# Kernel tuning notes

Hardware: AMD Instinct MI355X
Metric: run time of the kernel (lower is better)

## Reference

```python
import jax, jax.numpy as jnp
import numpy as np

WINDOW = 4  # window_size
H = 8       # n_heads


def setup_inputs() -> dict:
    key = jax.random.key(0)
    ks = jax.random.split(key, 12)
    B, C, T = 4, 512, 1024
    d = C // H
    x = jax.random.normal(ks[0], (B, C, T), dtype=jnp.float32)
    mask = jnp.ones((B, 1, 1, T), dtype=jnp.int32)
    s = 0.02
    Wq = jax.random.normal(ks[1], (C, C), dtype=jnp.float32) * s
    Wk = jax.random.normal(ks[2], (C, C), dtype=jnp.float32) * s
    Wv = jax.random.normal(ks[3], (C, C), dtype=jnp.float32) * s
    Wo = jax.random.normal(ks[4], (C, C), dtype=jnp.float32) * s
    bq = jnp.zeros((C,), jnp.float32)
    bk = jnp.zeros((C,), jnp.float32)
    bv = jnp.zeros((C,), jnp.float32)
    bo = jnp.zeros((C,), jnp.float32)
    rel_std = d ** (-0.5)
    emb_rel_k = jax.random.normal(ks[5], (1, 2 * WINDOW + 1, d), dtype=jnp.float32) * rel_std
    emb_rel_v = jax.random.normal(ks[6], (1, 2 * WINDOW + 1, d), dtype=jnp.float32) * rel_std
    return {"x": x, "mask": mask, "Wq": Wq, "bq": bq, "Wk": Wk, "bk": bk,
            "Wv": Wv, "bv": bv, "Wo": Wo, "bo": bo,
            "emb_rel_k": emb_rel_k, "emb_rel_v": emb_rel_v}


def _slice_rel_emb(emb, T, pad_len, start, end):
    # F.pad(emb, [0,0,pad,pad,0,0]) then [:, start:end] -> [1, 2T-1, d]
    p = jnp.pad(emb, ((0, 0), (pad_len, pad_len), (0, 0)))
    return p[:, start:end]


def reference(x, mask, Wq, bq, Wk, bk, Wv, bv, Wo, bo, emb_rel_k, emb_rel_v):
    B, C, T = x.shape
    d = C // H
    scale = jnp.asarray(np.sqrt(d), x.dtype)

    def proj(Wm, bm):
        return jnp.einsum('oc,bct->bot', Wm, x) + bm[None, :, None]

    def to_heads(t):  # [B,C,T] -> [B,H,T,d]
        return t.reshape(B, H, d, T).transpose(0, 1, 3, 2)

    query = to_heads(proj(Wq, bq))
    key_ = to_heads(proj(Wk, bk))
    value = to_heads(proj(Wv, bv))

    score = jnp.einsum('bhtd,bhsd->bhts', query, key_) / scale

    pad_len = max(0, T - (WINDOW + 1))
    start = max(0, WINDOW + 1 - T)
    end = start + 2 * T - 1

    k_emb = _slice_rel_emb(emb_rel_k, T, pad_len, start, end)  # [1, 2T-1, d]
    rel = jnp.einsum('bhtd,rd->bhtr', query, k_emb[0])          # [B,H,T,2T-1]
    # skew trick: relative -> absolute
    rel = jnp.pad(rel, ((0, 0), (0, 0), (0, 0), (0, 1))).reshape(B, H, 2 * T * T)
    rel = jnp.pad(rel, ((0, 0), (0, 0), (0, T - 1))).reshape(B, H, T + 1, 2 * T - 1)
    score_loc = rel[:, :, :T, T - 1:] / scale
    score = score + score_loc

    score = jnp.where(mask == 0, jnp.asarray(-10000.0, score.dtype), score)
    p_attn = jax.nn.softmax(score, axis=-1)  # dropout=0 (eval)

    output = jnp.einsum('bhts,bhsd->bhtd', p_attn, value)

    # inverse skew: absolute -> relative weights [B,H,T,2T-1]
    pw = jnp.pad(p_attn, ((0, 0), (0, 0), (0, 0), (0, T - 1))).reshape(B, H, T * (2 * T - 1))
    pw = jnp.pad(pw, ((0, 0), (0, 0), (T, 0))).reshape(B, H, T, 2 * T)[:, :, :, 1:]
    v_emb = _slice_rel_emb(emb_rel_v, T, pad_len, start, end)  # [1, 2T-1, d]
    output = output + jnp.einsum('bhtr,rd->bhtd', pw, v_emb[0])

    out = output.transpose(0, 1, 3, 2).reshape(B, C, T)
    return jnp.einsum('oc,bct->bot', Wo, out) + bo[None, :, None]
```

## Files before the change

kernel.cpp:

```cpp
#include <hip/hip_runtime.h>

typedef unsigned short u16;
typedef unsigned int u32;
using f32x4 = __attribute__((ext_vector_type(4))) float;
using s16x8 = __attribute__((ext_vector_type(8))) short;
using u16x4 = __attribute__((ext_vector_type(4))) unsigned short;
using u16x8 = __attribute__((ext_vector_type(8))) unsigned short;

#define GLOAD_LDS16(g, s)                                     \
  __builtin_amdgcn_global_load_lds(                           \
      (const __attribute__((address_space(1))) void*)(g),     \
      (__attribute__((address_space(3))) void*)(s), 16, 0, 0)

namespace {

constexpr int T = 1024;
constexpr int C = 512;
constexpr float QSCALE = 0.125f * 1.4426950408889634f;
constexpr float MASKED = -14427.0f;
constexpr float DEFER_THR = 11.0f;

__device__ inline u16 f2bf(float f) {
  u32 u = __builtin_bit_cast(u32, f);
  u32 r = (u + 0x7fffu + ((u >> 16) & 1u)) >> 16;
  return (u16)r;
}
__device__ inline float bf2f(u16 v) {
  return __builtin_bit_cast(float, (u32)v << 16);
}
__device__ inline f32x4 mfma16(s16x8 a, s16x8 b, f32x4 c) {
  return __builtin_amdgcn_mfma_f32_16x16x32_bf16(a, b, c, 0, 0, 0);
}
__device__ inline u32 cvtpk(float lo, float hi) {
  u32 r;
  asm("v_cvt_pk_bf16_f32 %0, %1, %2" : "=v"(r) : "v"(lo), "v"(hi));
  return r;
}

__global__ __launch_bounds__(256) void convert_all(
    const float* __restrict__ x, const float* __restrict__ Wq,
    const float* __restrict__ Wk, const float* __restrict__ Wv,
    const float* __restrict__ Wo, u16* __restrict__ xb, u16* __restrict__ Wqb,
    u16* __restrict__ Wkb, u16* __restrict__ Wvb, u16* __restrict__ Wob) {
  const int tid = threadIdx.x;
  const int bid = blockIdx.x;
  const float* src;
  u16* dst;
  size_t off;
  if (bid < 2048) {
    src = x; dst = xb;
    off = ((size_t)bid * 256 + tid) * 4;
  } else {
    const int j = bid - 2048;
    const int w = j >> 8;
    src = w == 0 ? Wq : w == 1 ? Wk : w == 2 ? Wv : Wo;
    dst = w == 0 ? Wqb : w == 1 ? Wkb : w == 2 ? Wvb : Wob;
    off = (((size_t)(j & 255)) * 256 + tid) * 4;
  }
  const float4 v = *reinterpret_cast<const float4*>(src + off);
  u16x4 o;
  o[0] = f2bf(v.x); o[1] = f2bf(v.y); o[2] = f2bf(v.z); o[3] = f2bf(v.w);
  *reinterpret_cast<u16x4*>(dst + off) = o;
}

__global__ __launch_bounds__(256) void qkv_gemm(
    const u16* __restrict__ xb, const u16* __restrict__ Wqb,
    const u16* __restrict__ Wkb, const u16* __restrict__ Wvb,
    const float* __restrict__ bq, const float* __restrict__ bk,
    const float* __restrict__ bv, u16* __restrict__ qb, u16* __restrict__ kswz,
    u16* __restrict__ vswz) {
  __shared__ u16 Bs[2][128 * 32];
  __shared__ float sbias[64];
  const int tid = threadIdx.x;
  const int z = blockIdx.z;
  const int b = z / 3, wsel = z - 3 * b;
  const u16* W = wsel == 0 ? Wqb : wsel == 1 ? Wkb : Wvb;
  const float* bias = wsel == 0 ? bq : wsel == 1 ? bk : bv;
  const int o0 = blockIdx.y * 64;
  const int t0 = blockIdx.x * 128;
  if (tid < 16)
    *reinterpret_cast<float4*>(&sbias[tid * 4]) =
        *reinterpret_cast<const float4*>(&bias[o0 + tid * 4]);

  const int l = tid & 63, wid = tid >> 6;
  const int wm = wid >> 1, wn = wid & 1;
  const int lr = l & 15, lg = l >> 4;

  const int cpair = tid & 15, tgrp = tid >> 4;
  const u16* xrow =
      xb + ((size_t)(b * C) + 2 * cpair) * T + t0 + 8 * tgrp;

  const u16* Arow0 = W + (size_t)(o0 + 32 * wm + lr) * C + 8 * lg;
  const u16* Arow1 = Arow0 + 16 * C;

  f32x4 acc[2][4] = {};

  auto stage = [&](int kk, int buf) {
    const u16* p = xrow + (size_t)kk * 32 * T;
    const u16x8 v0 = *reinterpret_cast<const u16x8*>(p);
    const u16x8 v1 = *reinterpret_cast<const u16x8*>(p + T);
    char* base = (char*)&Bs[buf][0];
#pragma unroll
    for (int j = 0; j < 8; ++j) {
      const int t = 8 * tgrp + j;
      const u32 w2 = (u32)v0[j] | ((u32)v1[j] << 16);
      *(u32*)(base + ((t * 64 + 4 * cpair) ^ ((t & 3) << 4))) = w2;
    }
  };

  s16x8 a0 = *reinterpret_cast<const s16x8*>(Arow0);
  s16x8 a1 = *reinterpret_cast<const s16x8*>(Arow1);
  stage(0, 0);
  __syncthreads();

  for (int kk = 0; kk < 16; ++kk) {
    s16x8 an0, an1;
    if (kk < 15) {
      an0 = *reinterpret_cast<const s16x8*>(Arow0 + (kk + 1) * 32);
      an1 = *reinterpret_cast<const s16x8*>(Arow1 + (kk + 1) * 32);
      stage(kk + 1, (kk + 1) & 1);
    }
    const char* rb = (const char*)&Bs[kk & 1][0];
#pragma unroll
    for (int nf = 0; nf < 4; ++nf) {
      const int t = 64 * wn + 16 * nf + lr;
      const s16x8 bfrag = *reinterpret_cast<const s16x8*>(
          rb + ((t * 64 + 16 * lg) ^ ((t & 3) << 4)));
      acc[0][nf] = mfma16(a0, bfrag, acc[0][nf]);
      acc[1][nf] = mfma16(a1, bfrag, acc[1][nf]);
    }
    __syncthreads();
    if (kk < 15) { a0 = an0; a1 = an1; }
  }

  const int h = o0 >> 6;
  const size_t bh = (size_t)(b * 8 + h);
  if (wsel == 0) {
#pragma unroll
    for (int m = 0; m < 2; ++m) {
      const int ob = 32 * wm + 16 * m + 4 * lg;
#pragma unroll
      for (int nf = 0; nf < 4; ++nf) {
        const int t = t0 + 64 * wn + 16 * nf + lr;
        u16x4 pk;
#pragma unroll
        for (int r = 0; r < 4; ++r)
          pk[r] = f2bf((acc[m][nf][r] + sbias[ob + r]) * QSCALE);
        *reinterpret_cast<u16x4*>(&qb[(bh * T + t) * 64 + ob]) = pk;
      }
    }
  } else if (wsel == 1) {
    char* kbase = (char*)kswz;
#pragma unroll
    for (int m = 0; m < 2; ++m) {
      const int ob = 32 * wm + 16 * m + 4 * lg;
#pragma unroll
      for (int nf = 0; nf < 4; ++nf) {
        const int t = t0 + 64 * wn + 16 * nf + lr;
        const int tile = t >> 6, row = t & 63;
        u16x4 pk;
#pragma unroll
        for (int r = 0; r < 4; ++r) pk[r] = f2bf(acc[m][nf][r] + sbias[ob + r]);
        const int off = (row * 128 + 2 * ob) ^ ((row & 7) << 4);
        *(u16x4*)(kbase + (bh * 16 + tile) * 8192 + off) = pk;
      }
    }
  } else {
    char* vbase = (char*)vswz;
#pragma unroll
    for (int m = 0; m < 2; ++m) {
      const int ob = 32 * wm + 16 * m + 4 * lg;
#pragma unroll
      for (int nf = 0; nf < 4; ++nf) {
        const int t = t0 + 64 * wn + 16 * nf + lr;
        const int tile = t >> 6, col2 = 2 * (t & 63);
#pragma unroll
        for (int r = 0; r < 4; ++r) {
          const int dd = ob + r;
          const int off = (dd * 128 + col2) ^ ((dd & 7) << 4);
          *(u16*)(vbase + (bh * 16 + tile) * 8192 + off) =
              f2bf(acc[m][nf][r] + sbias[dd]);
        }
      }
    }
  }
}

__global__ __launch_bounds__(512) void attn_swapped(
    const u16* __restrict__ qb, const u16* __restrict__ kswz,
    const u16* __restrict__ vswz, const int* __restrict__ gmask,
    const float* __restrict__ ek, const float* __restrict__ ev,
    u16* __restrict__ op0, u16* __restrict__ op1, float2* __restrict__ mlb) {
  __shared__ u16 Kbuf[2][8192];
  __shared__ u16 Vbuf[2][8192];
  __shared__ u16 Pdiag[8][256];
  __shared__ float rkk[128][12];
  __shared__ float eks[9][64];
  __shared__ float evs[9][64];
  __shared__ u16 zerobuf[16];
  __shared__ int tflag[16];

  const int p = blockIdx.x + 8 * blockIdx.y + 64 * blockIdx.z;
  const int xcd = p & 7;
  const int slot = p >> 3;
  const int zz = xcd;
  const int h = slot >> 3;
  const int tcx = slot & 7;
  const int b = zz >> 1, shalf = zz & 1;
  const int tc = tcx * 128;

  const int tid = threadIdx.x;
  const int l = tid & 63, wid = tid >> 6;
  const int lr = l & 15, lg = l >> 4;

  const size_t bh = (size_t)(b * 8 + h);
  const u16* qbh = qb + bh * T * 64;
  const u16* kimg0 = kswz + bh * 65536;
  const u16* vimg0 = vswz + bh * 65536;

  if (tid < 144) {
    reinterpret_cast<float4*>(&eks[0][0])[tid] =
        reinterpret_cast<const float4*>(ek)[tid];
    reinterpret_cast<float4*>(&evs[0][0])[tid] =
        reinterpret_cast<const float4*>(ev)[tid];
  }
  if (tid < 16) { tflag[tid] = 1; zerobuf[tid] = 0; }
  __syncthreads();

  auto stage_pair = [&](int stp, int buf) {
    const u16* ki = kimg0 + (size_t)stp * 4096;
    const u16* vi = vimg0 + (size_t)stp * 4096;
#pragma unroll
    for (int j = 0; j < 2; ++j) {
      const int seg = wid + 8 * j;
      GLOAD_LDS16(ki + seg * 512 + l * 8, &Kbuf[buf][seg * 512]);
      GLOAD_LDS16(vi + seg * 512 + l * 8, &Vbuf[buf][seg * 512]);
    }
  };
  const int st0 = shalf * 8;
  stage_pair(st0, 0);

  if (tid < 256) {
    const int4 mm = reinterpret_cast<const int4*>(gmask + b * T)[tid];
    if (!(mm.x && mm.y && mm.z && mm.w)) tflag[tid >> 4] = 0;
  }

  {
    const int r = tid >> 2, sub = tid & 3;
    const u16* qp = qbh + (size_t)(tc + r) * 64 + sub * 16;
    const u16x8 q0 = *reinterpret_cast<const u16x8*>(qp);
    const u16x8 q1 = *reinterpret_cast<const u16x8*>(qp + 8);
    float qf[16];
#pragma unroll
    for (int j = 0; j < 8; ++j) {
      qf[j] = bf2f(q0[j]);
      qf[j + 8] = bf2f(q1[j]);
    }
    float part[9];
#pragma unroll
    for (int w = 0; w < 9; ++w) {
      float s = 0.f;
      const float* er = &eks[w][sub * 16];
#pragma unroll
      for (int d = 0; d < 16; ++d) s += qf[d] * er[d];
      part[w] = s;
    }
#pragma unroll
    for (int w = 0; w < 9; ++w) {
      part[w] += __shfl_xor(part[w], 1);
      part[w] += __shfl_xor(part[w], 2);
    }
    if (sub == 0) {
#pragma unroll
      for (int w = 0; w < 9; ++w) rkk[r][w] = part[w];
    }
  }

  const int tbw = tc + 16 * wid;
  const int qg = tbw + lr;
  s16x8 aq0, aq1;
  {
    const u16* qgp = qbh + (size_t)qg * 64;
    aq0 = *reinterpret_cast<const s16x8*>(qgp + 8 * lg);
    aq1 = *reinterpret_cast<const s16x8*>(qgp + 32 + 8 * lg);
  }

  s16x8 evA[4];
#pragma unroll
  for (int nf = 0; nf < 4; ++nf) {
    const int dd = 16 * nf + lr;
#pragma unroll
    for (int e = 0; e < 8; ++e) {
      float v = 0.f;
      if (lg == 0) v = evs[e][dd];
      else if (lg == 1 && e == 0) v = evs[8][dd];
      evA[nf][e] = (short)f2bf(v);
    }
  }

  float m = -1e30f, lsum = 0.f;
  f32x4 Oa[4] = {};
  u16* Pd = &Pdiag[wid][0];

  __syncthreads();

  auto redist = [&](const f32x4* St, s16x8& pv0, s16x8& pv1) {
    u32 wpk[4][2];
#pragma unroll
    for (int nf = 0; nf < 4; ++nf) {
      wpk[nf][0] = cvtpk(St[nf][0], St[nf][1]);
      wpk[nf][1] = cvtpk(St[nf][2], St[nf][3]);
    }
    const int srcLo = lr + ((lg & 1) << 5);
    const int srcHi = srcLo + 16;
    const bool hiSel = (lg >> 1) != 0;
    union { u32 u[4]; s16x8 v; } pa0, pa1;
    {
      const u32 a0_ = __shfl((int)wpk[0][0], srcLo), b0_ = __shfl((int)wpk[1][0], srcLo);
      const u32 a1_ = __shfl((int)wpk[0][1], srcLo), b1_ = __shfl((int)wpk[1][1], srcLo);
      const u32 a2_ = __shfl((int)wpk[0][0], srcHi), b2_ = __shfl((int)wpk[1][0], srcHi);
      const u32 a3_ = __shfl((int)wpk[0][1], srcHi), b3_ = __shfl((int)wpk[1][1], srcHi);
      pa0.u[0] = hiSel ? b0_ : a0_; pa0.u[1] = hiSel ? b1_ : a1_;
      pa0.u[2] = hiSel ? b2_ : a2_; pa0.u[3] = hiSel ? b3_ : a3_;
    }
    {
      const u32 a0_ = __shfl((int)wpk[2][0], srcLo), b0_ = __shfl((int)wpk[3][0], srcLo);
      const u32 a1_ = __shfl((int)wpk[2][1], srcLo), b1_ = __shfl((int)wpk[3][1], srcLo);
      const u32 a2_ = __shfl((int)wpk[2][0], srcHi), b2_ = __shfl((int)wpk[3][0], srcHi);
      const u32 a3_ = __shfl((int)wpk[2][1], srcHi), b3_ = __shfl((int)wpk[3][1], srcHi);
      pa1.u[0] = hiSel ? b0_ : a0_; pa1.u[1] = hiSel ? b1_ : a1_;
      pa1.u[2] = hiSel ? b2_ : a2_; pa1.u[3] = hiSel ? b3_ : a3_;
    }
    pv0 = pa0.v;
    pv1 = pa1.v;
  };

  int cur = 0;
  for (int ii = 0; ii < 4; ++ii) {
    const int stp = st0 + 2 * ii;
    const int s0 = stp * 64, s1 = s0 + 64;
    if (ii < 3) stage_pair(stp + 2, cur ^ 1);

    f32x4 StA[4] = {}, StB[4] = {};
    const char* ksb = (const char*)&Kbuf[cur][0];
#pragma unroll
    for (int nf = 0; nf < 4; ++nf) {
      const int srow = 16 * nf + lr;
      const int swz = (srow & 7) << 4;
      const int o0_ = (srow * 128 + 16 * lg) ^ swz;
      const int o1_ = (srow * 128 + 16 * (lg + 4)) ^ swz;
      const s16x8 ka0 = *reinterpret_cast<const s16x8*>(ksb + o0_);
      const s16x8 ka1 = *reinterpret_cast<const s16x8*>(ksb + o1_);
      const s16x8 kb0 = *reinterpret_cast<const s16x8*>(ksb + 8192 + o0_);
      const s16x8 kb1 = *reinterpret_cast<const s16x8*>(ksb + 8192 + o1_);
      StA[nf] = mfma16(ka0, aq0, StA[nf]);
      StB[nf] = mfma16(kb0, aq0, StB[nf]);
      StA[nf] = mfma16(ka1, aq1, StA[nf]);
      StB[nf] = mfma16(kb1, aq1, StB[nf]);
    }

    const bool diagA = (s0 <= tbw + 19) && (s0 + 63 >= tbw - 4);
    const bool diagB = (s1 <= tbw + 19) && (s1 + 63 >= tbw - 4);

    if (diagA) {
#pragma unroll
      for (int nf = 0; nf < 4; ++nf)
#pragma unroll
        for (int r = 0; r < 4; ++r) {
          const int sd = (s0 + 16 * nf + 4 * lg + r) - qg;
          if (sd >= -4 && sd <= 4) StA[nf][r] += rkk[16 * wid + lr][sd + 4];
        }
    }
    if (diagB) {
#pragma unroll
      for (int nf = 0; nf < 4; ++nf)
#pragma unroll
        for (int r = 0; r < 4; ++r) {
          const int sd = (s1 + 16 * nf + 4 * lg + r) - qg;
          if (sd >= -4 && sd <= 4) StB[nf][r] += rkk[16 * wid + lr][sd + 4];
        }
    }
    if (!tflag[stp]) {
#pragma unroll
      for (int nf = 0; nf < 4; ++nf)
#pragma unroll
        for (int r = 0; r < 4; ++r)
          if (gmask[b * T + s0 + 16 * nf + 4 * lg + r] == 0) StA[nf][r] = MASKED;
    }
    if (!tflag[stp + 1]) {
#pragma unroll
      for (int nf = 0; nf < 4; ++nf)
#pragma unroll
        for (int r = 0; r < 4; ++r)
          if (gmask[b * T + s1 + 16 * nf + 4 * lg + r] == 0) StB[nf][r] = MASKED;
    }

    float rm;
    {
      float mv = fmaxf(fmaxf(StA[0][0], StA[0][1]), fmaxf(StA[0][2], StA[0][3]));
#pragma unroll
      for (int nf = 1; nf < 4; ++nf)
        mv = fmaxf(mv, fmaxf(fmaxf(StA[nf][0], StA[nf][1]),
                             fmaxf(StA[nf][2], StA[nf][3])));
#pragma unroll
      for (int nf = 0; nf < 4; ++nf)
        mv = fmaxf(mv, fmaxf(fmaxf(StB[nf][0], StB[nf][1]),
                             fmaxf(StB[nf][2], StB[nf][3])));
      rm = mv;
      rm = fmaxf(rm, __shfl_xor(rm, 16));
      rm = fmaxf(rm, __shfl_xor(rm, 32));
    }
    if (!__all(rm - m <= DEFER_THR)) {
      const float mn = fmaxf(m, rm);
      const float corr = exp2f(m - mn);
#pragma unroll
      for (int nf = 0; nf < 4; ++nf) {
        Oa[nf][0] *= corr; Oa[nf][1] *= corr;
        Oa[nf][2] *= corr; Oa[nf][3] *= corr;
      }
      lsum *= corr;
      m = mn;
    }
    float rs = 0.f;
#pragma unroll
    for (int nf = 0; nf < 4; ++nf)
#pragma unroll
      for (int r = 0; r < 4; ++r) {
        const float pA = exp2f(StA[nf][r] - m);
        const float pB = exp2f(StB[nf][r] - m);
        StA[nf][r] = pA;
        StB[nf][r] = pB;
        rs += pA + pB;
      }
    rs += __shfl_xor(rs, 16);
    rs += __shfl_xor(rs, 32);
    lsum += rs;

    const bool diagP = diagA || diagB;
    if (diagP) {
      u32* pz = (u32*)Pd;
      pz[l] = 0; pz[l + 64] = 0;
      if (diagA) {
#pragma unroll
        for (int nf = 0; nf < 4; ++nf)
#pragma unroll
          for (int r = 0; r < 4; ++r) {
            const int sd = (s0 + 16 * nf + 4 * lg + r) - qg;
            if (sd >= -4 && sd <= 4) Pd[lr * 16 + sd + 4] = f2bf(StA[nf][r]);
          }
      }
      if (diagB) {
#pragma unroll
        for (int nf = 0; nf < 4; ++nf)
#pragma unroll
          for (int r = 0; r < 4; ++r) {
            const int sd = (s1 + 16 * nf + 4 * lg + r) - qg;
            if (sd >= -4 && sd <= 4) Pd[lr * 16 + sd + 4] = f2bf(StB[nf][r]);
          }
      }
    }

    const char* vsb = (const char*)&Vbuf[cur][0];
    {
      s16x8 pa0, pa1;
      redist(StA, pa0, pa1);
#pragma unroll
      for (int nf = 0; nf < 4; ++nf) {
        const int dd = 16 * nf + lr;
        const int swz = (dd & 7) << 4;
        const s16x8 bv0 = *reinterpret_cast<const s16x8*>(
            vsb + ((dd * 128 + 16 * lg) ^ swz));
        const s16x8 bv1 = *reinterpret_cast<const s16x8*>(
            vsb + ((dd * 128 + 16 * (lg + 4)) ^ swz));
        Oa[nf] = mfma16(bv0, pa0, Oa[nf]);
        Oa[nf] = mfma16(bv1, pa1, Oa[nf]);
      }
    }
    {
      s16x8 pa0, pa1;
      redist(StB, pa0, pa1);
#pragma unroll
      for (int nf = 0; nf < 4; ++nf) {
        const int dd = 16 * nf + lr;
        const int swz = (dd & 7) << 4;
        const s16x8 bv0 = *reinterpret_cast<const s16x8*>(
            vsb + 8192 + ((dd * 128 + 16 * lg) ^ swz));
        const s16x8 bv1 = *reinterpret_cast<const s16x8*>(
            vsb + 8192 + ((dd * 128 + 16 * (lg + 4)) ^ swz));
        Oa[nf] = mfma16(bv0, pa0, Oa[nf]);
        Oa[nf] = mfma16(bv1, pa1, Oa[nf]);
      }
    }

    if (diagP) {
      const u16* pdsrc = (lg < 2) ? &Pd[lr * 16 + 8 * lg] : &zerobuf[0];
      const s16x8 pd = *reinterpret_cast<const s16x8*>(pdsrc);
#pragma unroll
      for (int nf = 0; nf < 4; ++nf) Oa[nf] = mfma16(evA[nf], pd, Oa[nf]);
    }

    __syncthreads();
    cur ^= 1;
  }

  u16* op = shalf ? op1 : op0;
#pragma unroll
  for (int nf = 0; nf < 4; ++nf) {
    u16x4 pk;
#pragma unroll
    for (int r = 0; r < 4; ++r) pk[r] = f2bf(Oa[nf][r]);
    *reinterpret_cast<u16x4*>(
        &op[(bh * T + qg) * 64 + 16 * nf + 4 * lg]) = pk;
  }
  if (lg == 0) {
    float2 v;
    v.x = m;
    v.y = lsum;
    mlb[(size_t)shalf * 32768 + bh * T + qg] = v;
  }
}

__global__ __launch_bounds__(256) void merge_halves(
    const u16* __restrict__ op0, const u16* __restrict__ op1,
    const float2* __restrict__ mlb, u16* __restrict__ attb) {
  const int tid = threadIdx.x;
  const int row = blockIdx.x * 16 + (tid >> 4);
  const int dd = (tid & 15) * 4;
  const float2 ml0 = mlb[row];
  const float2 ml1 = mlb[32768 + row];
  const float mm = fmaxf(ml0.x, ml1.x);
  const float a0 = exp2f(ml0.x - mm), a1 = exp2f(ml1.x - mm);
  const float inv = 1.0f / (a0 * ml0.y + a1 * ml1.y);
  const u16x4 v0 = *reinterpret_cast<const u16x4*>(&op0[(size_t)row * 64 + dd]);
  const u16x4 v1 = *reinterpret_cast<const u16x4*>(&op1[(size_t)row * 64 + dd]);
  u16x4 o;
#pragma unroll
  for (int j = 0; j < 4; ++j)
    o[j] = f2bf((bf2f(v0[j]) * a0 + bf2f(v1[j]) * a1) * inv);
  *reinterpret_cast<u16x4*>(&attb[(size_t)row * 64 + dd]) = o;
}

__global__ __launch_bounds__(256) void out_gemm(
    const u16* __restrict__ Wob, const float* __restrict__ bo,
    const u16* __restrict__ attb, float* __restrict__ out) {
  __shared__ u16 Bs[2][128 * 32];
  __shared__ float sbias[64];
  const int tid = threadIdx.x;
  const int b = blockIdx.z;
  const int o0 = blockIdx.y * 64;
  const int t0 = blockIdx.x * 128;
  if (tid < 16)
    *reinterpret_cast<float4*>(&sbias[tid * 4]) =
        *reinterpret_cast<const float4*>(&bo[o0 + tid * 4]);

  const int l = tid & 63, wid = tid >> 6;
  const int wm = wid >> 1, wn = wid & 1;
  const int lr = l & 15, lg = l >> 4;

  const int slot = tid & 3, trow = tid >> 2;
  const u16* Arow0 = Wob + (size_t)(o0 + 32 * wm + lr) * C + 8 * lg;
  const u16* Arow1 = Arow0 + 16 * C;

  f32x4 acc[2][4] = {};

  auto stage = [&](int kk, int buf) {
    const int c0 = kk * 32;
    const int h = c0 >> 6, dd0 = c0 & 63;
    char* base = (char*)&Bs[buf][0];
#pragma unroll
    for (int rep = 0; rep < 2; ++rep) {
      const int t = rep * 64 + trow;
      const u16x8 v = *reinterpret_cast<const u16x8*>(
          &attb[((size_t)((b * 8 + h) * T) + t0 + t) * 64 + dd0 + 8 * slot]);
      *(u16x8*)(base + ((t * 64 + 16 * slot) ^ ((t & 3) << 4))) = v;
    }
  };

  s16x8 a0 = *reinterpret_cast<const s16x8*>(Arow0);
  s16x8 a1 = *reinterpret_cast<const s16x8*>(Arow1);
  stage(0, 0);
  __syncthreads();

  for (int kk = 0; kk < 16; ++kk) {
    s16x8 an0, an1;
    if (kk < 15) {
      an0 = *reinterpret_cast<const s16x8*>(Arow0 + (kk + 1) * 32);
      an1 = *reinterpret_cast<const s16x8*>(Arow1 + (kk + 1) * 32);
      stage(kk + 1, (kk + 1) & 1);
    }
    const char* rb = (const char*)&Bs[kk & 1][0];
#pragma unroll
    for (int nf = 0; nf < 4; ++nf) {
      const int t = 64 * wn + 16 * nf + lr;
      const s16x8 bfrag = *reinterpret_cast<const s16x8*>(
          rb + ((t * 64 + 16 * lg) ^ ((t & 3) << 4)));
      acc[0][nf] = mfma16(a0, bfrag, acc[0][nf]);
      acc[1][nf] = mfma16(a1, bfrag, acc[1][nf]);
    }
    __syncthreads();
    if (kk < 15) { a0 = an0; a1 = an1; }
  }

#pragma unroll
  for (int m = 0; m < 2; ++m) {
    const int ol = 32 * wm + 16 * m + 4 * lg;
#pragma unroll
    for (int nf = 0; nf < 4; ++nf) {
      const int t = t0 + 64 * wn + 16 * nf + lr;
#pragma unroll
      for (int r = 0; r < 4; ++r)
        out[((size_t)(b * C) + o0 + ol + r) * T + t] =
            acc[m][nf][r] + sbias[ol + r];
    }
  }
}

}

extern "C" void kernel_launch(void* const* d_in, const int* in_sizes, int n_in,
                              void* d_out, int out_size, void* d_ws,
                              size_t ws_size, hipStream_t stream) {
  const float* x    = (const float*)d_in[0];
  const int*   mask = (const int*)d_in[1];
  const float* Wq   = (const float*)d_in[2];
  const float* bq   = (const float*)d_in[3];
  const float* Wk   = (const float*)d_in[4];
  const float* bk   = (const float*)d_in[5];
  const float* Wv   = (const float*)d_in[6];
  const float* bv   = (const float*)d_in[7];
  const float* Wo   = (const float*)d_in[8];
  const float* bo   = (const float*)d_in[9];
  const float* ek   = (const float*)d_in[10];
  const float* ev   = (const float*)d_in[11];
  float* out = (float*)d_out;

  char* ws = (char*)d_ws;
  u16* xb   = (u16*)(ws);
  u16* Wqb  = (u16*)(ws + 4194304);
  u16* Wkb  = (u16*)(ws + 4718592);
  u16* Wvb  = (u16*)(ws + 5242880);
  u16* Wob  = (u16*)(ws + 5767168);
  u16* qb   = (u16*)(ws + 6291456);
  u16* kswz = (u16*)(ws + 10485760);
  u16* vswz = (u16*)(ws + 14680064);
  u16* attb = (u16*)(ws + 18874368);
  u16* op0  = xb;
  u16* op1  = (u16*)(ws + 23068672);
  float2* mlb = (float2*)(ws + 27262976);

  convert_all<<<dim3(3072), dim3(256), 0, stream>>>(x, Wq, Wk, Wv, Wo, xb, Wqb,
                                                    Wkb, Wvb, Wob);
  qkv_gemm<<<dim3(8, 8, 12), dim3(256), 0, stream>>>(xb, Wqb, Wkb, Wvb, bq, bk,
                                                     bv, qb, kswz, vswz);
  attn_swapped<<<dim3(8, 8, 8), dim3(512), 0, stream>>>(
      qb, kswz, vswz, mask, ek, ev, op0, op1, mlb);
  merge_halves<<<dim3(2048), dim3(256), 0, stream>>>(op0, op1, mlb, attb);
  out_gemm<<<dim3(8, 8, 4), dim3(256), 0, stream>>>(Wob, bo, attb, out);
}
```

Before: 80.10 us.

## Read K/V fragments directly from global memory instead of LDS double-buffering

Removes the shared-memory double buffers for K and V tiles along with the async global-to-LDS staging and the per-iteration block barrier. MFMA operands are now loaded straight from the pre-swizzled global K/V images, relying on L1/L2 caching since all 8 waves read the same tiles. This cuts 64KB of LDS use and the sync points, which may allow higher occupancy. The trade-off is exposed global load latency with no prefetch and more redundant L2 traffic per wave.

```diff
diff --git a/kernel.cpp b/kernel.cpp
--- a/kernel.cpp
+++ b/kernel.cpp
@@ -6,11 +6,6 @@
 using s16x8 = __attribute__((ext_vector_type(8))) short;
 using u16x4 = __attribute__((ext_vector_type(4))) unsigned short;
 using u16x8 = __attribute__((ext_vector_type(8))) unsigned short;
-
-#define GLOAD_LDS16(g, s)                                     \
-  __builtin_amdgcn_global_load_lds(                           \
-      (const __attribute__((address_space(1))) void*)(g),     \
-      (__attribute__((address_space(3))) void*)(s), 16, 0, 0)
 
 namespace {
 
@@ -191,8 +186,6 @@
     const u16* __restrict__ vswz, const int* __restrict__ gmask,
     const float* __restrict__ ek, const float* __restrict__ ev,
     u16* __restrict__ op0, u16* __restrict__ op1, float2* __restrict__ mlb) {
-  __shared__ u16 Kbuf[2][8192];
-  __shared__ u16 Vbuf[2][8192];
   __shared__ u16 Pdiag[8][256];
   __shared__ float rkk[128][12];
   __shared__ float eks[9][64];
@@ -226,19 +219,6 @@
   }
   if (tid < 16) { tflag[tid] = 1; zerobuf[tid] = 0; }
   __syncthreads();
-
-  auto stage_pair = [&](int stp, int buf) {
-    const u16* ki = kimg0 + (size_t)stp * 4096;
-    const u16* vi = vimg0 + (size_t)stp * 4096;
-#pragma unroll
-    for (int j = 0; j < 2; ++j) {
-      const int seg = wid + 8 * j;
-      GLOAD_LDS16(ki + seg * 512 + l * 8, &Kbuf[buf][seg * 512]);
-      GLOAD_LDS16(vi + seg * 512 + l * 8, &Vbuf[buf][seg * 512]);
-    }
-  };
-  const int st0 = shalf * 8;
-  stage_pair(st0, 0);
 
   if (tid < 256) {
     const int4 mm = reinterpret_cast<const int4*>(gmask + b * T)[tid];
@@ -335,24 +315,24 @@
     pv1 = pa1.v;
   };
 
-  int cur = 0;
+  const int st0 = shalf * 8;
   for (int ii = 0; ii < 4; ++ii) {
     const int stp = st0 + 2 * ii;
     const int s0 = stp * 64, s1 = s0 + 64;
-    if (ii < 3) stage_pair(stp + 2, cur ^ 1);
+    const char* kA = (const char*)(kimg0 + (size_t)stp * 4096);
+    const char* vA = (const char*)(vimg0 + (size_t)stp * 4096);
 
     f32x4 StA[4] = {}, StB[4] = {};
-    const char* ksb = (const char*)&Kbuf[cur][0];
 #pragma unroll
     for (int nf = 0; nf < 4; ++nf) {
       const int srow = 16 * nf + lr;
       const int swz = (srow & 7) << 4;
       const int o0_ = (srow * 128 + 16 * lg) ^ swz;
       const int o1_ = (srow * 128 + 16 * (lg + 4)) ^ swz;
-      const s16x8 ka0 = *reinterpret_cast<const s16x8*>(ksb + o0_);
-      const s16x8 ka1 = *reinterpret_cast<const s16x8*>(ksb + o1_);
-      const s16x8 kb0 = *reinterpret_cast<const s16x8*>(ksb + 8192 + o0_);
-      const s16x8 kb1 = *reinterpret_cast<const s16x8*>(ksb + 8192 + o1_);
+      const s16x8 ka0 = *reinterpret_cast<const s16x8*>(kA + o0_);
+      const s16x8 ka1 = *reinterpret_cast<const s16x8*>(kA + o1_);
+      const s16x8 kb0 = *reinterpret_cast<const s16x8*>(kA + 8192 + o0_);
+      const s16x8 kb1 = *reinterpret_cast<const s16x8*>(kA + 8192 + o1_);
       StA[nf] = mfma16(ka0, aq0, StA[nf]);
       StB[nf] = mfma16(kb0, aq0, StB[nf]);
       StA[nf] = mfma16(ka1, aq1, StA[nf]);
@@ -460,7 +440,6 @@
       }
     }
 
-    const char* vsb = (const char*)&Vbuf[cur][0];
     {
       s16x8 pa0, pa1;
       redist(StA, pa0, pa1);
@@ -469,9 +448,9 @@
         const int dd = 16 * nf + lr;
         const int swz = (dd & 7) << 4;
         const s16x8 bv0 = *reinterpret_cast<const s16x8*>(
-            vsb + ((dd * 128 + 16 * lg) ^ swz));
+            vA + ((dd * 128 + 16 * lg) ^ swz));
         const s16x8 bv1 = *reinterpret_cast<const s16x8*>(
-            vsb + ((dd * 128 + 16 * (lg + 4)) ^ swz));
+            vA + ((dd * 128 + 16 * (lg + 4)) ^ swz));
         Oa[nf] = mfma16(bv0, pa0, Oa[nf]);
         Oa[nf] = mfma16(bv1, pa1, Oa[nf]);
       }
@@ -484,9 +463,9 @@
         const int dd = 16 * nf + lr;
         const int swz = (dd & 7) << 4;
         const s16x8 bv0 = *reinterpret_cast<const s16x8*>(
-            vsb + 8192 + ((dd * 128 + 16 * lg) ^ swz));
+            vA + 8192 + ((dd * 128 + 16 * lg) ^ swz));
         const s16x8 bv1 = *reinterpret_cast<const s16x8*>(
-            vsb + 8192 + ((dd * 128 + 16 * (lg + 4)) ^ swz));
+            vA + 8192 + ((dd * 128 + 16 * (lg + 4)) ^ swz));
         Oa[nf] = mfma16(bv0, pa0, Oa[nf]);
         Oa[nf] = mfma16(bv1, pa1, Oa[nf]);
       }
@@ -498,9 +477,6 @@
 #pragma unroll
       for (int nf = 0; nf < 4; ++nf) Oa[nf] = mfma16(evA[nf], pd, Oa[nf]);
     }
-
-    __syncthreads();
-    cur ^= 1;
   }
 
   u16* op = shalf ? op1 : op0;
```

Measured after the change: 98.60 us. +23.1%, slower.
